# Optimization experiments

Measured on AMD Instinct MI355X. Metric: run time of the kernel, lower is better.

Reference implementation:

```python
import jax, jax.numpy as jnp
import numpy as np

SCALE = 0.125  # 1/sqrt(D_head=64)
NEG_INF = -1.0e9


def setup_inputs() -> dict:
    key = jax.random.key(0)
    kq, kk, kv, km = jax.random.split(key, 4)
    B, L, N, D = 2, 2048, 16, 64
    query = jax.random.normal(kq, (B, L, N, D), dtype=jnp.float32)
    k = jax.random.normal(kk, (B, L, N, D), dtype=jnp.float32)
    v = jax.random.normal(kv, (B, L, N, D), dtype=jnp.float32)
    attn_mask = jax.random.randint(km, (B, L, L), 0, 2).astype(jnp.bool_)
    return {"query": query, "key": k, "value": v, "attn_mask": attn_mask}


def reference(query, key, value, attn_mask):
    # scores: [B, L_q, L_k, N]
    attention = jnp.einsum('bind,bjnd->bijn', query, key) * SCALE
    # mask broadcast over heads; True positions are masked out
    attention = jnp.where(attn_mask[:, :, :, None], NEG_INF, attention)
    # softmax over the key axis (dim=2), dropout p=0.0 is identity
    attention = jax.nn.softmax(attention, axis=2)
    context = jnp.einsum('bijn,bjnd->bind', attention, value)
    return (context, attention)
```

## Files before the change

### kernel.cpp

```cpp
#include <hip/hip_runtime.h>
#include <hip/hip_bf16.h>

typedef unsigned short u16;
typedef unsigned char u8;
typedef __attribute__((ext_vector_type(8))) short bf16x8;
typedef __attribute__((ext_vector_type(4))) float f32x4;

#define MFMA16(a, b, c) __builtin_amdgcn_mfma_f32_16x16x32_bf16(a, b, c, 0, 0, 0)

#define LGKM_BARRIER()                                     \
    do {                                                   \
        asm volatile("s_waitcnt lgkmcnt(0)" ::: "memory"); \
        __builtin_amdgcn_s_barrier();                      \
        asm volatile("" ::: "memory");                     \
    } while (0)

static __device__ __forceinline__ u16 f2bf(float f) {
    __hip_bfloat16 h = __float2bfloat16(f);
    return *reinterpret_cast<u16*>(&h);
}
static __device__ __forceinline__ float bf2f(u16 h) {
    unsigned u = ((unsigned)h) << 16;
    return __uint_as_float(u);
}

__global__ __launch_bounds__(256) void kconv_kernel(const float* __restrict__ kf,
                                                    u16* __restrict__ kb) {
    const size_t i = ((size_t)blockIdx.x * 256 + threadIdx.x) * 4;
    float4 f = *(const float4*)(kf + i);
    alignas(8) u16 w[4] = {f2bf(f.x), f2bf(f.y), f2bf(f.z), f2bf(f.w)};
    *(uint2*)(kb + i) = *(const uint2*)w;
}

__global__ __launch_bounds__(256) void vt_kernel(const float* __restrict__ v,
                                                 u16* __restrict__ vt) {
    __shared__ u16 T[64][72];
    const int t = threadIdx.x, bid = blockIdx.x;
    const int b = bid >> 9, n = bid & 15, j0 = ((bid >> 4) & 31) << 6;
    {
        const int jj = t >> 4, tt = t & 15;
#pragma unroll
        for (int rep = 0; rep < 4; rep++) {
            const int j = rep * 16 + jj;
            const float* src = v + (((size_t)((b * 2048 + j0 + j) * 16 + n)) << 6) + tt * 4;
            float4 f = *(const float4*)src;
            alignas(8) u16 w[4] = {f2bf(f.x), f2bf(f.y), f2bf(f.z), f2bf(f.w)};
            *(uint2*)&T[j][tt * 4] = *(const uint2*)w;
        }
    }
    __syncthreads();
    {
        const int d = t >> 2, jq = t & 3;
        alignas(16) u16 w[16];
#pragma unroll
        for (int e = 0; e < 16; e++) w[e] = T[jq * 16 + e][d];
        u16* dst = vt + (((size_t)((b * 16 + n) * 64 + d)) << 11) + j0 + jq * 16;
        *(uint4*)dst = *(const uint4*)&w[0];
        *(uint4*)(dst + 8) = *(const uint4*)&w[8];
    }
}

__global__ __launch_bounds__(1024, 4) void attn_kernel(
    const float* __restrict__ qf, const u16* __restrict__ kb_g,
    const u16* __restrict__ vt, const void* __restrict__ mask,
    float* __restrict__ ctx, float* __restrict__ attn) {
    __shared__ u16 maskT[2048];
    __shared__ u16 pbuf[2][16][16][40];

    const int tid = threadIdx.x;
    const int lane = tid & 63;
    const int wv = tid >> 6;
    const int g = lane >> 4, c = lane & 15;
    const int rbit = g * 4;

    const int bid = blockIdx.x;
    const int b = ((bid & 7) < 4) ? 0 : 1;
    const int idx = ((bid >> 3) << 2) | (bid & 3);
    const int i0 = idx << 4;

    bool mask_is_u8;
    {
        unsigned acc = 0;
        const unsigned* mw = (const unsigned*)mask;
#pragma unroll
        for (int i = 0; i < 64; i++) acc |= mw[i];
        mask_is_u8 = (acc & 0xFFFFFF00u) != 0u;
    }

    {
        const size_t base = ((size_t)(b * 2048 + i0)) * 2048 + (size_t)tid * 2;
        unsigned m0 = 0, m1 = 0;
        if (mask_is_u8) {
            const u8* m8 = (const u8*)mask;
#pragma unroll
            for (int i = 0; i < 16; i++) {
                const u8* mp = m8 + base + (size_t)i * 2048;
                if (mp[0]) m0 |= (1u << i);
                if (mp[1]) m1 |= (1u << i);
            }
        } else {
            const int* m32 = (const int*)mask;
#pragma unroll
            for (int i = 0; i < 16; i++) {
                const int* mp = m32 + base + (size_t)i * 2048;
                if (mp[0]) m0 |= (1u << i);
                if (mp[1]) m1 |= (1u << i);
            }
        }
        *reinterpret_cast<unsigned*>(&maskT[tid * 2]) = m0 | (m1 << 16);
    }
    __syncthreads();

    bf16x8 aq0, aq1;
    {
        const float* qp = qf + (((size_t)(b * 2048 + i0 + c) * 16 + wv) << 6) + g * 8;
        float4 f0 = *(const float4*)qp;
        float4 f1 = *(const float4*)(qp + 4);
        float4 f2 = *(const float4*)(qp + 32);
        float4 f3 = *(const float4*)(qp + 36);
        alignas(16) u16 w0[8] = {f2bf(f0.x), f2bf(f0.y), f2bf(f0.z), f2bf(f0.w),
                                 f2bf(f1.x), f2bf(f1.y), f2bf(f1.z), f2bf(f1.w)};
        alignas(16) u16 w1[8] = {f2bf(f2.x), f2bf(f2.y), f2bf(f2.z), f2bf(f2.w),
                                 f2bf(f3.x), f2bf(f3.y), f2bf(f3.z), f2bf(f3.w)};
        aq0 = *(const bf16x8*)w0;
        aq1 = *(const bf16x8*)w1;
    }

    const u16* kb = kb_g + (((size_t)(b * 2048) * 16 + wv) << 6) + g * 8;
    const u16* vb = vt + (((size_t)(b * 16 + wv)) << 17);

    float l0 = 0.f, l1 = 0.f, l2 = 0.f, l3 = 0.f;
    for (int j0 = 0; j0 < 2048; j0 += 16) {
        const u16* kp = kb + (size_t)(j0 + c) * 1024;
        bf16x8 b0 = *(const bf16x8*)kp;
        bf16x8 b1 = *(const bf16x8*)(kp + 32);
        f32x4 s = {0.f, 0.f, 0.f, 0.f};
        s = MFMA16(aq0, b0, s);
        s = MFMA16(aq1, b1, s);
        const unsigned mt = maskT[j0 + c];
        l0 += __expf(((mt >> (rbit + 0)) & 1) ? -1e9f : s[0] * 0.125f);
        l1 += __expf(((mt >> (rbit + 1)) & 1) ? -1e9f : s[1] * 0.125f);
        l2 += __expf(((mt >> (rbit + 2)) & 1) ? -1e9f : s[2] * 0.125f);
        l3 += __expf(((mt >> (rbit + 3)) & 1) ? -1e9f : s[3] * 0.125f);
    }
#pragma unroll
    for (int off = 1; off <= 8; off <<= 1) {
        l0 += __shfl_xor(l0, off);
        l1 += __shfl_xor(l1, off);
        l2 += __shfl_xor(l2, off);
        l3 += __shfl_xor(l3, off);
    }
    const float n0i = (l0 != 0.f) ? 1.f / l0 : 0.f;
    const float n1i = (l1 != 0.f) ? 1.f / l1 : 0.f;
    const float n2i = (l2 != 0.f) ? 1.f / l2 : 0.f;
    const float n3i = (l3 != 0.f) ? 1.f / l3 : 0.f;

    f32x4 o0 = {0.f, 0.f, 0.f, 0.f}, o1 = o0, o2 = o0, o3 = o0;

    const int wo_i = tid >> 6;
    const int wo_c = tid & 63;
    const int wo_j = wo_c >> 1;
    const int wo_n = (wo_c & 1) << 3;
    float* attn_row = attn + (((size_t)(b * 2048 + i0 + wo_i)) << 15) + wo_n;

    bf16x8 ck0a, ck0b, ck1a, ck1b, cv0, cv1, cv2, cv3;
    {
        const u16* kp0 = kb + (size_t)c * 1024;
        ck0a = *(const bf16x8*)kp0;
        ck0b = *(const bf16x8*)(kp0 + 32);
        const u16* kp1 = kb + (size_t)(16 + c) * 1024;
        ck1a = *(const bf16x8*)kp1;
        ck1b = *(const bf16x8*)(kp1 + 32);
        const u16* vp = vb + (size_t)c * 2048 + g * 8;
        cv0 = *(const bf16x8*)(vp);
        cv1 = *(const bf16x8*)(vp + 16 * 2048);
        cv2 = *(const bf16x8*)(vp + 32 * 2048);
        cv3 = *(const bf16x8*)(vp + 48 * 2048);
    }

    int p = 0;
    for (int j0 = 0; j0 < 2048; j0 += 32, p ^= 1) {
        {
            f32x4 s = {0.f, 0.f, 0.f, 0.f};
            s = MFMA16(aq0, ck0a, s);
            s = MFMA16(aq1, ck0b, s);
            const unsigned mt = maskT[j0 + c];
            pbuf[p][wv][rbit + 0][c] =
                f2bf(__expf(((mt >> (rbit + 0)) & 1) ? -1e9f : s[0] * 0.125f) * n0i);
            pbuf[p][wv][rbit + 1][c] =
                f2bf(__expf(((mt >> (rbit + 1)) & 1) ? -1e9f : s[1] * 0.125f) * n1i);
            pbuf[p][wv][rbit + 2][c] =
                f2bf(__expf(((mt >> (rbit + 2)) & 1) ? -1e9f : s[2] * 0.125f) * n2i);
            pbuf[p][wv][rbit + 3][c] =
                f2bf(__expf(((mt >> (rbit + 3)) & 1) ? -1e9f : s[3] * 0.125f) * n3i);
        }
        {
            f32x4 s = {0.f, 0.f, 0.f, 0.f};
            s = MFMA16(aq0, ck1a, s);
            s = MFMA16(aq1, ck1b, s);
            const unsigned mt = maskT[j0 + 16 + c];
            pbuf[p][wv][rbit + 0][16 + c] =
                f2bf(__expf(((mt >> (rbit + 0)) & 1) ? -1e9f : s[0] * 0.125f) * n0i);
            pbuf[p][wv][rbit + 1][16 + c] =
                f2bf(__expf(((mt >> (rbit + 1)) & 1) ? -1e9f : s[1] * 0.125f) * n1i);
            pbuf[p][wv][rbit + 2][16 + c] =
                f2bf(__expf(((mt >> (rbit + 2)) & 1) ? -1e9f : s[2] * 0.125f) * n2i);
            pbuf[p][wv][rbit + 3][16 + c] =
                f2bf(__expf(((mt >> (rbit + 3)) & 1) ? -1e9f : s[3] * 0.125f) * n3i);
        }
        LGKM_BARRIER();

        const bf16x8 ap = *(const bf16x8*)&pbuf[p][wv][c][g * 8];

        const int jn = (j0 + 32) & 2047;
        bf16x8 nk0a, nk0b, nk1a, nk1b, nv0, nv1, nv2, nv3;
        {
            const u16* kp0 = kb + (size_t)(jn + c) * 1024;
            nk0a = *(const bf16x8*)kp0;
            nk0b = *(const bf16x8*)(kp0 + 32);
            const u16* kp1 = kb + (size_t)(jn + 16 + c) * 1024;
            nk1a = *(const bf16x8*)kp1;
            nk1b = *(const bf16x8*)(kp1 + 32);
            const u16* vp = vb + (size_t)c * 2048 + jn + g * 8;
            nv0 = *(const bf16x8*)(vp);
            nv1 = *(const bf16x8*)(vp + 16 * 2048);
            nv2 = *(const bf16x8*)(vp + 32 * 2048);
            nv3 = *(const bf16x8*)(vp + 48 * 2048);
        }

        o0 = MFMA16(ap, cv0, o0);
        o1 = MFMA16(ap, cv1, o1);
        o2 = MFMA16(ap, cv2, o2);
        o3 = MFMA16(ap, cv3, o3);

        __builtin_amdgcn_sched_barrier(0);

        {
            alignas(16) float w[8];
#pragma unroll
            for (int e = 0; e < 8; e++) w[e] = bf2f(pbuf[p][wo_n + e][wo_i][wo_j]);
            float* dst = attn_row + (size_t)(j0 + wo_j) * 16;
            *(f32x4*)dst = *(const f32x4*)&w[0];
            *(f32x4*)(dst + 4) = *(const f32x4*)&w[4];
        }

        ck0a = nk0a; ck0b = nk0b; ck1a = nk1a; ck1b = nk1b;
        cv0 = nv0; cv1 = nv1; cv2 = nv2; cv3 = nv3;
    }

#pragma unroll
    for (int r = 0; r < 4; r++) {
        float* cp = ctx + (((size_t)(b * 2048 + i0 + rbit + r) * 16 + wv) << 6) + c;
        cp[0]  = o0[r];
        cp[16] = o1[r];
        cp[32] = o2[r];
        cp[48] = o3[r];
    }
}

extern "C" void kernel_launch(void* const* d_in, const int* in_sizes, int n_in,
                              void* d_out, int out_size, void* d_ws, size_t ws_size,
                              hipStream_t stream) {
    const float* q   = (const float*)d_in[0];
    const float* k   = (const float*)d_in[1];
    const float* v   = (const float*)d_in[2];
    const void* mask = (const void*)d_in[3];

    float* ctx  = (float*)d_out;
    float* attn = (float*)d_out + 4194304;

    u16* vt = (u16*)d_ws;
    u16* kb = vt + 4194304;

    kconv_kernel<<<4096, 256, 0, stream>>>(k, kb);
    vt_kernel<<<1024, 256, 0, stream>>>(v, vt);
    attn_kernel<<<256, 1024, 0, stream>>>(q, kb, vt, mask, ctx, attn);
}
```

Before: 960.3 us.

## Split key range across two blocks per query tile and reduce partial contexts

Each query tile is now handled by two blocks, each covering half of the key axis. Each block writes its attention slice and a partial context to workspace, and a new reduce kernel sums the two partials into the output context. This doubles the grid so more of the device is busy, and the launch bound is raised accordingly. The cost is an extra kernel launch and extra traffic for the partial buffers. Any per-row normalization pass over all keys is also repeated by both blocks.

Measured after the change: 1.460 ms. +52.1%, slower.

```diff
diff --git a/kernel.cpp b/kernel.cpp
--- a/kernel.cpp
+++ b/kernel.cpp
@@ -60,10 +60,19 @@
     }
 }
 
-__global__ __launch_bounds__(1024, 4) void attn_kernel(
+__global__ __launch_bounds__(256) void ctx_reduce_kernel(const float* __restrict__ part,
+                                                         float* __restrict__ ctx) {
+    const size_t i = ((size_t)blockIdx.x * 256 + threadIdx.x) * 4;
+    f32x4 a = *(const f32x4*)(part + i);
+    f32x4 b = *(const f32x4*)(part + 4194304 + i);
+    f32x4 r = a + b;
+    *(f32x4*)(ctx + i) = r;
+}
+
+__global__ __launch_bounds__(1024, 8) void attn_kernel(
     const float* __restrict__ qf, const u16* __restrict__ kb_g,
     const u16* __restrict__ vt, const void* __restrict__ mask,
-    float* __restrict__ ctx, float* __restrict__ attn) {
+    float* __restrict__ part, float* __restrict__ attn) {
     __shared__ u16 maskT[2048];
     __shared__ u16 pbuf[2][16][16][40];
 
@@ -74,9 +83,12 @@
     const int rbit = g * 4;
 
     const int bid = blockIdx.x;
-    const int b = ((bid & 7) < 4) ? 0 : 1;
-    const int idx = ((bid >> 3) << 2) | (bid & 3);
+    const int xcd = bid & 7;
+    const int b = (xcd < 4) ? 0 : 1;
+    const int jh = (bid >> 3) & 1;
+    const int idx = ((bid >> 4) << 2) | (bid & 3);
     const int i0 = idx << 4;
+    const int jbase = jh << 10;
 
     bool mask_is_u8;
     {
@@ -165,13 +177,13 @@
 
     bf16x8 ck0a, ck0b, ck1a, ck1b, cv0, cv1, cv2, cv3;
     {
-        const u16* kp0 = kb + (size_t)c * 1024;
+        const u16* kp0 = kb + (size_t)(jbase + c) * 1024;
         ck0a = *(const bf16x8*)kp0;
         ck0b = *(const bf16x8*)(kp0 + 32);
-        const u16* kp1 = kb + (size_t)(16 + c) * 1024;
+        const u16* kp1 = kb + (size_t)(jbase + 16 + c) * 1024;
         ck1a = *(const bf16x8*)kp1;
         ck1b = *(const bf16x8*)(kp1 + 32);
-        const u16* vp = vb + (size_t)c * 2048 + g * 8;
+        const u16* vp = vb + (size_t)c * 2048 + jbase + g * 8;
         cv0 = *(const bf16x8*)(vp);
         cv1 = *(const bf16x8*)(vp + 16 * 2048);
         cv2 = *(const bf16x8*)(vp + 32 * 2048);
@@ -179,7 +191,7 @@
     }
 
     int p = 0;
-    for (int j0 = 0; j0 < 2048; j0 += 32, p ^= 1) {
+    for (int j0 = jbase; j0 < jbase + 1024; j0 += 32, p ^= 1) {
         {
             f32x4 s = {0.f, 0.f, 0.f, 0.f};
             s = MFMA16(aq0, ck0a, s);
@@ -250,7 +262,8 @@
 
 #pragma unroll
     for (int r = 0; r < 4; r++) {
-        float* cp = ctx + (((size_t)(b * 2048 + i0 + rbit + r) * 16 + wv) << 6) + c;
+        float* cp = part + ((size_t)jh << 22) +
+                    (((size_t)(b * 2048 + i0 + rbit + r) * 16 + wv) << 6) + c;
         cp[0]  = o0[r];
         cp[16] = o1[r];
         cp[32] = o2[r];
@@ -271,8 +284,10 @@
 
     u16* vt = (u16*)d_ws;
     u16* kb = vt + 4194304;
+    float* part = (float*)(kb + 4194304);
 
     kconv_kernel<<<4096, 256, 0, stream>>>(k, kb);
     vt_kernel<<<1024, 256, 0, stream>>>(v, vt);
-    attn_kernel<<<256, 1024, 0, stream>>>(q, kb, vt, mask, ctx, attn);
-}
+    attn_kernel<<<512, 1024, 0, stream>>>(q, kb, vt, mask, part, attn);
+    ctx_reduce_kernel<<<4096, 256, 0, stream>>>(part, ctx);
+}
```
